# Performance work log

Hardware: AMD Instinct MI355X
Metric: run time of the kernel (lower is better)

The kernel has to match this reference:

```python
import jax, jax.numpy as jnp
import numpy as np

DIM = 256  # channel width
B, H, W = 4, 64, 64


def conv2d(x, w, b, pad, groups=1):
    # x: NCHW, w: OIHW (I = C_in/groups)
    y = jax.lax.conv_general_dilated(
        x, w, window_strides=(1, 1),
        padding=[(pad[0], pad[0]), (pad[1], pad[1])],
        dimension_numbers=("NCHW", "OIHW", "NCHW"),
        feature_group_count=groups)
    return y + b[None, :, None, None]


def l2norm(x, eps=1e-12):
    # matches F.normalize(x, dim=-1): x / max(||x||_2, eps)
    n = jnp.sqrt(jnp.sum(x * x, axis=-1, keepdims=True))
    return x / jnp.maximum(n, eps)


def setup_inputs() -> dict:
    key = jax.random.key(0)
    ks = jax.random.split(key, 12)
    dim, c8 = DIM, DIM // 8
    w = lambda k, shape, s: jax.random.normal(k, shape, jnp.float32) * s
    return {
        "x": jax.random.normal(ks[0], (B, dim, H, W), jnp.float32),
        "w_conv": w(ks[1], (dim, dim, 3, 3), 0.02), "b_conv": jnp.zeros((dim,), jnp.float32),
        "w01": w(ks[2], (dim, 1, 1, 7), 0.05), "b01": jnp.zeros((dim,), jnp.float32),
        "w02": w(ks[3], (dim, 1, 7, 1), 0.05), "b02": jnp.zeros((dim,), jnp.float32),
        "w11": w(ks[4], (dim, 1, 1, 11), 0.05), "b11": jnp.zeros((dim,), jnp.float32),
        "w12": w(ks[5], (dim, 1, 11, 1), 0.05), "b12": jnp.zeros((dim,), jnp.float32),
        "w21": w(ks[6], (dim, 1, 1, 21), 0.05), "b21": jnp.zeros((dim,), jnp.float32),
        "w22": w(ks[7], (dim, 1, 21, 1), 0.05), "b22": jnp.zeros((dim,), jnp.float32),
        "w_proj": w(ks[8], (c8, dim, 1, 1), 0.05), "b_proj": jnp.zeros((c8,), jnp.float32),
        "w3": w(ks[9], (c8, dim // 4, 1, 1), 0.05), "b3": jnp.zeros((c8,), jnp.float32),
        "w4": w(ks[10], (dim, c8, 1, 1), 0.05), "b4": jnp.zeros((dim,), jnp.float32),
    }


def reference(x, w_conv, b_conv, w01, b01, w02, b02, w11, b11, w12, b12,
              w21, b21, w22, b22, w_proj, b_proj, w3, b3, w4, b4):
    b, c, h, w_ = x.shape
    x = conv2d(x, w_conv, b_conv, (1, 1))
    # multi-scale separable depthwise convs (7, 11, 21)
    x1 = conv2d(conv2d(x, w01, b01, (0, 3), c), w02, b02, (3, 0), c)
    x2 = conv2d(conv2d(x, w11, b11, (0, 5), c), w12, b12, (5, 0), c)
    x3 = conv2d(conv2d(x, w21, b21, (0, 10), c), w22, b22, (10, 0), c)
    out1 = x1 + x2 + x3 + x                      # [b, dim, h, w]
    out1 = conv2d(out1, w_proj, b_proj, (0, 0))  # [b, dim//8, h, w]
    c8 = out1.shape[1]
    t = out1.reshape(b, c8, h * w_)              # b head c (h w), head=1

    q1 = l2norm(t)
    attn1 = jax.nn.softmax(q1 @ jnp.swapaxes(q1, -2, -1), axis=-1)  # [b, c8, c8]
    out2 = attn1 @ t                                                # [b, c8, hw]

    # branch 2: spatial attention (hw x hw)
    ts = jnp.swapaxes(t, -2, -1)                 # [b, hw, c8]
    q2 = l2norm(ts)
    attn2 = jax.nn.softmax(q2 @ jnp.swapaxes(q2, -2, -1), axis=-1)  # [b, hw, hw]
    out3 = jnp.swapaxes(attn2 @ ts, -2, -1)                         # [b, c8, hw]

    out4 = jnp.concatenate([out2.reshape(b, c8, h, w_),
                            out3.reshape(b, c8, h, w_)], axis=1)    # [b, dim//4, h, w]
    out5 = conv2d(out4, w3, b3, (0, 0)) + out1
    return conv2d(out5, w4, b4, (0, 0))          # [b, dim, h, w]
```

## Files before the change

kernel.cpp:

```cpp
#include <hip/hip_runtime.h>
#include <hip/hip_bf16.h>

typedef __hip_bfloat16 bf16;
typedef short s16;
typedef __attribute__((ext_vector_type(4))) short s16x4;
typedef __attribute__((ext_vector_type(8))) short s16x8;
typedef __attribute__((ext_vector_type(4))) float f32x4;

__device__ __forceinline__ s16 f2b(float f){
    unsigned u = __float_as_uint(f);
    unsigned r = (u + 0x7FFFu + ((u >> 16) & 1u)) >> 16;
    return (s16)r;
}
__device__ __forceinline__ float b2f_bits(s16 v){
    return __uint_as_float(((unsigned)(unsigned short)v) << 16);
}

__global__ __launch_bounds__(256) void prep_k(const float* __restrict__ x, s16* __restrict__ xcl,
                                              const float* __restrict__ w, s16* __restrict__ wpk){
    __shared__ s16 lb[64][258];
    int blk = blockIdx.x, t = threadIdx.x;
    if (blk < 256){
        int h = blk & 63, b = blk >> 6;
        for (int i = t; i < 16384; i += 256){
            int ci = i >> 6, ww = i & 63;
            lb[ww][ci] = f2b(x[((b*256 + ci)*64 + h)*64 + ww]);
        }
        __syncthreads();
        for (int i = t; i < 16384; i += 256){
            int ww = i >> 8, ci = i & 255;
            xcl[(b*4096 + h*64 + ww)*256 + ci] = lb[ww][ci];
        }
    } else {
        int base = (blk - 256)*1024 + t;
        #pragma unroll
        for (int k = 0; k < 4; ++k){
            int idx = base + k*256;
            int cil = idx & 31;
            int r   = idx >> 5;
            int co  = r & 255;
            int r2  = r >> 8;
            int tap = r2 % 9, cc = r2 / 9;
            wpk[idx] = f2b(w[(co*256 + cc*32 + cil)*9 + tap]);
        }
    }
}

__global__ __launch_bounds__(256) void conv3x3m_k(const s16* __restrict__ xcl,
        const s16* __restrict__ wpk, const float* __restrict__ bias,
        bf16* __restrict__ y0){
    __shared__ alignas(16) s16 smem[30240];
    s16* xls = smem;
    s16* wls = smem + 9504;
    const int sp = blockIdx.x, cog = blockIdx.y;
    const int b = sp >> 5, h0 = (sp & 31)*2;
    const int t = threadIdx.x;
    const int wv = t >> 6, lane = t & 63;
    const int lm = lane & 15, g = lane >> 4;

    f32x4 acc[2][4];
    #pragma unroll
    for (int mi = 0; mi < 2; ++mi)
        #pragma unroll
        for (int ni = 0; ni < 4; ++ni) acc[mi][ni] = (f32x4){0.f,0.f,0.f,0.f};

    for (int cc = 0; cc < 8; ++cc){
        __syncthreads();
        for (int i = t; i < 1056; i += 256){
            int g8 = i & 3, wi = (i>>2) % 66, r = (i>>2) / 66;
            int h = h0 - 1 + r, w = wi - 1;
            s16x8 v = {0,0,0,0,0,0,0,0};
            if (h >= 0 && h < 64 && w >= 0 && w < 64)
                v = *(const s16x8*)&xcl[(b*4096 + h*64 + w)*256 + cc*32 + g8*8];
            s16* d = &xls[(r*66 + wi)*36 + g8*8];
            *(s16x4*)d       = __builtin_shufflevector(v, v, 0,1,2,3);
            *(s16x4*)(d + 4) = __builtin_shufflevector(v, v, 4,5,6,7);
        }
        for (int i = t; i < 2304; i += 256){
            int g8 = i & 3, co = (i>>2) & 63, tap = i >> 8;
            s16x8 v = *(const s16x8*)&wpk[((cc*9 + tap)*256 + cog*64 + co)*32 + g8*8];
            s16* d = &wls[(tap*64 + co)*36 + g8*8];
            *(s16x4*)d       = __builtin_shufflevector(v, v, 0,1,2,3);
            *(s16x4*)(d + 4) = __builtin_shufflevector(v, v, 4,5,6,7);
        }
        __syncthreads();
        #pragma unroll
        for (int tap = 0; tap < 9; ++tap){
            const int kh = tap/3, kw = tap%3;
            s16x8 bfr[4], afr[2];
            #pragma unroll
            for (int ni = 0; ni < 4; ++ni){
                const s16* p = &wls[(tap*64 + ni*16 + lm)*36 + g*8];
                s16x4 lo = *(const s16x4*)p;
                s16x4 hi = *(const s16x4*)(p + 4);
                bfr[ni] = __builtin_shufflevector(lo, hi, 0,1,2,3,4,5,6,7);
            }
            #pragma unroll
            for (int mi = 0; mi < 2; ++mi){
                int m = (wv*2 + mi)*16 + lm;
                int hr = m >> 6, ww = m & 63;
                const s16* p = &xls[((hr + kh)*66 + (ww + kw))*36 + g*8];
                s16x4 lo = *(const s16x4*)p;
                s16x4 hi = *(const s16x4*)(p + 4);
                afr[mi] = __builtin_shufflevector(lo, hi, 0,1,2,3,4,5,6,7);
            }
            #pragma unroll
            for (int mi = 0; mi < 2; ++mi)
                #pragma unroll
                for (int ni = 0; ni < 4; ++ni)
                    acc[mi][ni] = __builtin_amdgcn_mfma_f32_16x16x32_bf16(
                        afr[mi], bfr[ni], acc[mi][ni], 0, 0, 0);
        }
    }
    __syncthreads();
    float* ot = (float*)smem;
    #pragma unroll
    for (int mi = 0; mi < 2; ++mi)
        #pragma unroll
        for (int ni = 0; ni < 4; ++ni)
            #pragma unroll
            for (int r = 0; r < 4; ++r){
                int m  = (wv*2 + mi)*16 + g*4 + r;
                int co = ni*16 + lm;
                ot[co*132 + m] = acc[mi][ni][r];
            }
    __syncthreads();
    for (int i = t; i < 8192; i += 256){
        int co = i >> 7, m = i & 127;
        float v = ot[co*132 + m] + bias[cog*64 + co];
        y0[((b*256 + cog*64 + co)*64 + h0 + (m>>6))*64 + (m & 63)] = __float2bfloat16(v);
    }
}

template<int K>
__device__ __forceinline__ void sep_branch(const float (*__restrict__ pl)[65], float (*__restrict__ hp)[65],
                                           int c, int t,
                                           const float* __restrict__ wh, const float* __restrict__ bh,
                                           const float* __restrict__ wv, const float* __restrict__ bv,
                                           float* acc){
    constexpr int P = K/2;
    constexpr int W = 16 + 2*P;
    float wk[K];
    #pragma unroll
    for (int j = 0; j < K; ++j) wk[j] = wh[c*K + j];
    float bhv = bh[c];
    {
        int h = t >> 2, w0 = (t & 3)*16;
        float win[W];
        #pragma unroll
        for (int j = 0; j < W; ++j){
            int ww = w0 - P + j;
            win[j] = (ww >= 0 && ww < 64) ? pl[h][ww] : 0.f;
        }
        __syncthreads();
        #pragma unroll
        for (int i = 0; i < 16; ++i){
            float s = bhv;
            #pragma unroll
            for (int k = 0; k < K; ++k) s += win[i+k]*wk[k];
            hp[h][w0 + i] = s;
        }
    }
    float vk[K];
    #pragma unroll
    for (int j = 0; j < K; ++j) vk[j] = wv[c*K + j];
    float bvv = bv[c];
    __syncthreads();
    {
        int w = t & 63, h0 = (t >> 6)*16;
        float win[W];
        #pragma unroll
        for (int j = 0; j < W; ++j){
            int hh = h0 - P + j;
            win[j] = (hh >= 0 && hh < 64) ? hp[hh][w] : 0.f;
        }
        #pragma unroll
        for (int i = 0; i < 16; ++i){
            float s = bvv;
            #pragma unroll
            for (int k = 0; k < K; ++k) s += win[i+k]*vk[k];
            acc[i] += s;
        }
    }
}

__global__ __launch_bounds__(256) void sepconv_k(const bf16* __restrict__ y0,
        const float* __restrict__ w01, const float* __restrict__ b01,
        const float* __restrict__ w02, const float* __restrict__ b02,
        const float* __restrict__ w11, const float* __restrict__ b11,
        const float* __restrict__ w12, const float* __restrict__ b12,
        const float* __restrict__ w21, const float* __restrict__ b21,
        const float* __restrict__ w22, const float* __restrict__ b22,
        bf16* __restrict__ out1){
    __shared__ float pl[64][65];
    __shared__ float hp[64][65];
    int bc = blockIdx.x;
    int c = bc & 255;
    int t = threadIdx.x;
    const s16* src = (const s16*)(y0 + bc*4096);
    #pragma unroll
    for (int k = 0; k < 2; ++k){
        int chunk = t + k*256;
        int h = chunk >> 3, w8 = (chunk & 7)*8;
        s16x8 v = *(const s16x8*)&src[h*64 + w8];
        #pragma unroll
        for (int e = 0; e < 8; ++e) pl[h][w8 + e] = b2f_bits(v[e]);
    }
    __syncthreads();
    float acc[16];
    #pragma unroll
    for (int k = 0; k < 16; ++k) acc[k] = 0.f;
    sep_branch<7 >(pl, hp, c, t, w01, b01, w02, b02, acc);
    sep_branch<11>(pl, hp, c, t, w11, b11, w12, b12, acc);
    sep_branch<21>(pl, hp, c, t, w21, b21, w22, b22, acc);
    __syncthreads();
    {
        int w = t & 63, h0 = (t >> 6)*16;
        #pragma unroll
        for (int i = 0; i < 16; ++i) hp[h0 + i][w] = acc[i] + pl[h0 + i][w];
    }
    __syncthreads();
    s16* dst = (s16*)(out1 + bc*4096);
    #pragma unroll
    for (int k = 0; k < 2; ++k){
        int chunk = t + k*256;
        int h = chunk >> 3, w8 = (chunk & 7)*8;
        s16x8 o;
        #pragma unroll
        for (int e = 0; e < 8; ++e) o[e] = f2b(hp[h][w8 + e]);
        *(s16x8*)&dst[h*64 + w8] = o;
    }
}

__global__ __launch_bounds__(256) void proj_k(const bf16* __restrict__ out1, const float* __restrict__ wp,
                                              const float* __restrict__ bp,
                                              s16* __restrict__ tTb, float* __restrict__ rn2){
    __shared__ float wl[256*32];
    __shared__ s16 part[4][64][36];
    int pt = blockIdx.x, b = blockIdx.y, t = threadIdx.x;
    int q = t >> 6, lane = t & 63;
    for (int i = t; i < 8192; i += 256){
        int ci = i >> 5, cc = i & 31;
        wl[ci*32 + cc] = wp[cc*256 + ci];
    }
    __syncthreads();
    int p = pt*64 + lane;
    float acc[32] = {};
    const bf16* xb = out1 + b*1048576 + p;
    for (int ci = q*64; ci < q*64 + 64; ++ci){
        float v = __bfloat162float(xb[ci*4096]);
        const float* wr = &wl[ci*32];
        #pragma unroll
        for (int c8 = 0; c8 < 8; ++c8){
            float4 w4 = *(const float4*)&wr[c8*4];
            acc[c8*4+0] += w4.x*v; acc[c8*4+1] += w4.y*v;
            acc[c8*4+2] += w4.z*v; acc[c8*4+3] += w4.w*v;
        }
    }
    #pragma unroll
    for (int cc = 0; cc < 32; ++cc) part[q][lane][cc] = f2b(acc[cc]);
    __syncthreads();
    int p_loc = t >> 2, qq = t & 3;
    int pg = pt*64 + p_loc;
    float a8[8];
    float ss = 0.f;
    #pragma unroll
    for (int c = 0; c < 8; ++c){
        int cc = qq*8 + c;
        float v = b2f_bits(part[0][p_loc][cc]) + b2f_bits(part[1][p_loc][cc])
                + b2f_bits(part[2][p_loc][cc]) + b2f_bits(part[3][p_loc][cc]) + bp[cc];
        a8[c] = v;
        ss += v*v;
    }
    ss += __shfl_xor(ss, 1, 4);
    ss += __shfl_xor(ss, 2, 4);
    if (qq == 0) rn2[b*4096 + pg] = 1.f / fmaxf(sqrtf(ss), 1e-12f);
    s16x8 o8;
    #pragma unroll
    for (int c = 0; c < 8; ++c) o8[c] = f2b(a8[c]);
    *(s16x8*)&tTb[(b*4096 + pg)*32 + qq*8] = o8;
}

__global__ __launch_bounds__(256) void gramm_k(const s16* __restrict__ tTb, float* __restrict__ part){
    __shared__ alignas(16) s16 ts[32*268];
    int ks = blockIdx.x, b = blockIdx.y, t = threadIdx.x;
    {
        const s16* src = &tTb[(b*4096 + ks*256 + t)*32];
        s16 row[32];
        #pragma unroll
        for (int q = 0; q < 4; ++q){
            s16x8 v = *(const s16x8*)&src[q*8];
            #pragma unroll
            for (int e = 0; e < 8; ++e) row[q*8 + e] = v[e];
        }
        #pragma unroll
        for (int cc = 0; cc < 32; ++cc) ts[cc*268 + t] = row[cc];
    }
    __syncthreads();
    int wv = t >> 6, lane = t & 63, lm = lane & 15, g = lane >> 4;
    int mi = wv >> 1, ni = wv & 1;
    f32x4 acc = (f32x4){0.f,0.f,0.f,0.f};
    const s16* ar = &ts[(mi*16 + lm)*268];
    const s16* br = &ts[(ni*16 + lm)*268];
    #pragma unroll
    for (int kk = 0; kk < 8; ++kk){
        const s16* ap = ar + kk*32 + g*8;
        s16x4 alo = *(const s16x4*)ap;
        s16x4 ahi = *(const s16x4*)(ap + 4);
        s16x8 af = __builtin_shufflevector(alo, ahi, 0,1,2,3,4,5,6,7);
        const s16* bp = br + kk*32 + g*8;
        s16x4 blo = *(const s16x4*)bp;
        s16x4 bhi = *(const s16x4*)(bp + 4);
        s16x8 bf = __builtin_shufflevector(blo, bhi, 0,1,2,3,4,5,6,7);
        acc = __builtin_amdgcn_mfma_f32_16x16x32_bf16(af, bf, acc, 0, 0, 0);
    }
    float* pd = part + (b*16 + ks)*1024;
    #pragma unroll
    for (int r = 0; r < 4; ++r){
        int i = mi*16 + g*4 + r, j = ni*16 + lm;
        pd[i*32 + j] = acc[r];
    }
}

__global__ __launch_bounds__(256) void afold_k(const float* __restrict__ part,
        const float* __restrict__ w3, const float* __restrict__ b3,
        const float* __restrict__ w4, const float* __restrict__ b4,
        float* __restrict__ WtT, float* __restrict__ WoT, float* __restrict__ bfo){
    __shared__ float rn[32];
    __shared__ float rsum[32];
    __shared__ float a1[1024];
    __shared__ float w3a[1024];
    __shared__ float w3bs[1024];
    int b = blockIdx.x, t = threadIdx.x;
    if (t < 32){
        float gjj = 0.f;
        #pragma unroll 8
        for (int ps = 0; ps < 16; ++ps) gjj += part[(b*16+ps)*1024 + t*33];
        rn[t] = 1.f / fmaxf(sqrtf(gjj), 1e-12f);
    }
    for (int idx = t; idx < 1024; idx += 256){
        int i = idx >> 5, j = idx & 31;
        w3bs[idx] = w3[i*64 + 32 + j];
    }
    __syncthreads();
    for (int e = t; e < 1024; e += 256){
        int i = e >> 5, j = e & 31;
        float gij = 0.f;
        #pragma unroll 8
        for (int ps = 0; ps < 16; ++ps) gij += part[(b*16+ps)*1024 + e];
        a1[e] = __expf(rn[i]*rn[j]*gij);
    }
    __syncthreads();
    if (t < 32){
        float s = 0.f;
        #pragma unroll 8
        for (int j = 0; j < 32; ++j) s += a1[t*32 + j];
        rsum[t] = 1.f / s;
    }
    __syncthreads();
    for (int e = t; e < 1024; e += 256) a1[e] *= rsum[e >> 5];
    __syncthreads();
    for (int idx = t; idx < 1024; idx += 256){
        int cc = idx >> 5, j = idx & 31;
        float s = 0.f;
        #pragma unroll 8
        for (int i = 0; i < 32; ++i) s += w3[cc*64 + i]*a1[i*32 + j];
        w3a[idx] = s;
    }
    __syncthreads();
    int co = t;
    float w4r[32];
    #pragma unroll
    for (int cc = 0; cc < 32; ++cc) w4r[cc] = w4[co*32 + cc];
    float bfv = b4[co];
    #pragma unroll
    for (int cc = 0; cc < 32; ++cc) bfv += w4r[cc]*b3[cc];
    bfo[b*256 + co] = bfv;
    for (int j = 0; j < 32; ++j){
        float st = w4r[j];
        float so = 0.f;
        #pragma unroll 8
        for (int cc = 0; cc < 32; ++cc){
            st += w4r[cc]*w3a[cc*32 + j];
            so += w4r[cc]*w3bs[cc*32 + j];
        }
        WtT[(b*32 + j)*256 + co] = st;
        WoT[(b*32 + j)*256 + co] = so;
    }
}

__global__ __launch_bounds__(256) void flashm_k(const s16* __restrict__ tTb, const float* __restrict__ rn2,
                                                float* __restrict__ partA, float* __restrict__ partL){
    __shared__ alignas(16) s16 kvb[128*36];
    __shared__ alignas(16) s16 vts[32*132];
    __shared__ alignas(16) s16 pls[4][16*132];
    __shared__ float rnj[128];
    __shared__ float ri[64];
    const int ib = blockIdx.x, b = blockIdx.y, chunk = blockIdx.z;
    const int t = threadIdx.x, wv = t >> 6, lane = t & 63;
    const int lm = lane & 15, g = lane >> 4;
    const int i0 = ib*64;

    if (t < 64) ri[t] = rn2[b*4096 + i0 + t];
    s16x8 qf = *(const s16x8*)&tTb[(b*4096 + i0 + wv*16 + lm)*32 + g*8];
    __syncthreads();
    float rni4[4];
    #pragma unroll
    for (int r = 0; r < 4; ++r) rni4[r] = ri[wv*16 + g*4 + r];

    f32x4 oacc[2];
    oacc[0] = (f32x4){0.f,0.f,0.f,0.f};
    oacc[1] = (f32x4){0.f,0.f,0.f,0.f};
    float lacc[4] = {0.f,0.f,0.f,0.f};
    s16* pw = pls[wv];

    for (int jt = chunk*8; jt < chunk*8 + 8; ++jt){
        const int j0 = jt*128;
        __syncthreads();
        for (int gi = t; gi < 512; gi += 256){
            int j = gi >> 2, g8 = gi & 3;
            s16x8 v = *(const s16x8*)&tTb[(b*4096 + j0 + j)*32 + g8*8];
            s16* d = &kvb[j*36 + g8*8];
            *(s16x4*)d       = __builtin_shufflevector(v, v, 0,1,2,3);
            *(s16x4*)(d + 4) = __builtin_shufflevector(v, v, 4,5,6,7);
            #pragma unroll
            for (int e = 0; e < 8; ++e) vts[(g8*8 + e)*132 + j] = v[e];
        }
        if (t < 128) rnj[t] = rn2[b*4096 + j0 + t];
        __syncthreads();
        #pragma unroll
        for (int nt = 0; nt < 8; ++nt){
            const s16* bp = &kvb[(nt*16 + lm)*36 + g*8];
            s16x4 blo = *(const s16x4*)bp;
            s16x4 bhi = *(const s16x4*)(bp + 4);
            s16x8 bf = __builtin_shufflevector(blo, bhi, 0,1,2,3,4,5,6,7);
            f32x4 s = __builtin_amdgcn_mfma_f32_16x16x32_bf16(qf, bf,
                        (f32x4){0.f,0.f,0.f,0.f}, 0, 0, 0);
            float rj = rnj[nt*16 + lm];
            #pragma unroll
            for (int r = 0; r < 4; ++r){
                float e = __expf(s[r]*rni4[r]*rj);
                lacc[r] += e;
                pw[(g*4 + r)*132 + nt*16 + lm] = f2b(e);
            }
        }
        #pragma unroll
        for (int ks = 0; ks < 4; ++ks){
            const s16* ap = &pw[lm*132 + ks*32 + g*8];
            s16x4 alo = *(const s16x4*)ap;
            s16x4 ahi = *(const s16x4*)(ap + 4);
            s16x8 af = __builtin_shufflevector(alo, ahi, 0,1,2,3,4,5,6,7);
            #pragma unroll
            for (int n2 = 0; n2 < 2; ++n2){
                const s16* vp = &vts[(n2*16 + lm)*132 + ks*32 + g*8];
                s16x4 vlo = *(const s16x4*)vp;
                s16x4 vhi = *(const s16x4*)(vp + 4);
                s16x8 vf = __builtin_shufflevector(vlo, vhi, 0,1,2,3,4,5,6,7);
                oacc[n2] = __builtin_amdgcn_mfma_f32_16x16x32_bf16(af, vf, oacc[n2], 0, 0, 0);
            }
        }
    }
    #pragma unroll
    for (int r = 0; r < 4; ++r){
        float v = lacc[r];
        v += __shfl_xor(v, 1, 16); v += __shfl_xor(v, 2, 16);
        v += __shfl_xor(v, 4, 16); v += __shfl_xor(v, 8, 16);
        lacc[r] = v;
    }
    const int base = (b*4 + chunk)*4096 + i0 + wv*16;
    #pragma unroll
    for (int n2 = 0; n2 < 2; ++n2)
        #pragma unroll
        for (int r = 0; r < 4; ++r)
            partA[(base + g*4 + r)*32 + n2*16 + lm] = oacc[n2][r];
    if (lm == 0){
        #pragma unroll
        for (int r = 0; r < 4; ++r) partL[base + g*4 + r] = lacc[r];
    }
}

__global__ __launch_bounds__(256) void finalfuse_k(const s16* __restrict__ tTb,
        const float* __restrict__ partA, const float* __restrict__ partL,
        const float* __restrict__ WtT, const float* __restrict__ WoT,
        const float* __restrict__ bfo, float* __restrict__ out){
    int pt = blockIdx.x, cog = blockIdx.y, b = blockIdx.z, t = threadIdx.x;
    int p = pt*256 + t;
    float l = 0.f;
    #pragma unroll
    for (int c = 0; c < 4; ++c) l += partL[(b*4 + c)*4096 + p];
    float inv = 1.f / l;
    float v3[32];
    #pragma unroll
    for (int q = 0; q < 8; ++q){
        float4 s0 = *(const float4*)&partA[((b*4 + 0)*4096 + p)*32 + q*4];
        float4 s1 = *(const float4*)&partA[((b*4 + 1)*4096 + p)*32 + q*4];
        float4 s2 = *(const float4*)&partA[((b*4 + 2)*4096 + p)*32 + q*4];
        float4 s3 = *(const float4*)&partA[((b*4 + 3)*4096 + p)*32 + q*4];
        v3[q*4+0] = (s0.x + s1.x + s2.x + s3.x)*inv;
        v3[q*4+1] = (s0.y + s1.y + s2.y + s3.y)*inv;
        v3[q*4+2] = (s0.z + s1.z + s2.z + s3.z)*inv;
        v3[q*4+3] = (s0.w + s1.w + s2.w + s3.w)*inv;
    }
    float vt[32];
    {
        const s16* tp = &tTb[(b*4096 + p)*32];
        #pragma unroll
        for (int q = 0; q < 4; ++q){
            s16x8 v = *(const s16x8*)&tp[q*8];
            #pragma unroll
            for (int e = 0; e < 8; ++e) vt[q*8 + e] = b2f_bits(v[e]);
        }
    }
    float acc[32];
    #pragma unroll
    for (int co = 0; co < 32; ++co) acc[co] = bfo[b*256 + cog*32 + co];
    for (int j = 0; j < 32; ++j){
        float vtj = vt[j];
        float vo  = v3[j];
        const float* wtr = WtT + (b*32 + j)*256 + cog*32;
        const float* wor = WoT + (b*32 + j)*256 + cog*32;
        #pragma unroll
        for (int co = 0; co < 32; ++co) acc[co] += wtr[co]*vtj + wor[co]*vo;
    }
    #pragma unroll
    for (int co = 0; co < 32; ++co)
        out[((b*256 + cog*32 + co)*4096) + p] = acc[co];
}

extern "C" void kernel_launch(void* const* d_in, const int* in_sizes, int n_in,
                              void* d_out, int out_size, void* d_ws, size_t ws_size,
                              hipStream_t stream) {
    const float* x      = (const float*)d_in[0];
    const float* w_conv = (const float*)d_in[1];
    const float* b_conv = (const float*)d_in[2];
    const float* w01 = (const float*)d_in[3];  const float* b01 = (const float*)d_in[4];
    const float* w02 = (const float*)d_in[5];  const float* b02 = (const float*)d_in[6];
    const float* w11 = (const float*)d_in[7];  const float* b11 = (const float*)d_in[8];
    const float* w12 = (const float*)d_in[9];  const float* b12 = (const float*)d_in[10];
    const float* w21 = (const float*)d_in[11]; const float* b21 = (const float*)d_in[12];
    const float* w22 = (const float*)d_in[13]; const float* b22 = (const float*)d_in[14];
    const float* w_proj = (const float*)d_in[15]; const float* b_proj = (const float*)d_in[16];
    const float* w3 = (const float*)d_in[17]; const float* b3 = (const float*)d_in[18];
    const float* w4 = (const float*)d_in[19]; const float* b4 = (const float*)d_in[20];

    char* wsb = (char*)d_ws;
    s16*   xcl  = (s16*)wsb;
    bf16*  out1 = (bf16*)wsb;
    bf16*  y0   = (bf16*)(wsb + 8388608);
    s16*   wpk  = (s16*)(wsb + 16777216);
    float* f    = (float*)d_ws;
    float* part   = f + 0;
    float* partA  = f + 0;
    s16*   tTb    = (s16*)(wsb + 10485760);
    float* WtT    = f + 3145728;
    float* WoT    = f + 3178496;
    float* bfo    = f + 3211264;
    float* partL  = f + 4194304;
    float* rn2    = f + 4726912;

    prep_k<<<dim3(832), 256, 0, stream>>>(x, xcl, w_conv, wpk);
    conv3x3m_k<<<dim3(128, 4), 256, 0, stream>>>(xcl, wpk, b_conv, y0);
    sepconv_k<<<dim3(1024), 256, 0, stream>>>(y0, w01, b01, w02, b02,
                                              w11, b11, w12, b12,
                                              w21, b21, w22, b22, out1);
    proj_k<<<dim3(64, 4), 256, 0, stream>>>(out1, w_proj, b_proj, tTb, rn2);
    gramm_k<<<dim3(16, 4), 256, 0, stream>>>(tTb, part);
    afold_k<<<dim3(4), 256, 0, stream>>>(part, w3, b3, w4, b4, WtT, WoT, bfo);
    flashm_k<<<dim3(64, 4, 4), 256, 0, stream>>>(tTb, rn2, partA, partL);
    finalfuse_k<<<dim3(16, 8, 4), 256, 0, stream>>>(tTb, partA, partL, WtT, WoT, bfo,
                                                    (float*)d_out);
}
```

Measured before the change: 297.1 us.

## Pre-pad conv input in global memory and read A fragments directly

Measured after the change: 305.9 us. +2.9%, slower.

```diff
diff --git a/kernel.cpp b/kernel.cpp
--- a/kernel.cpp
+++ b/kernel.cpp
@@ -16,7 +16,7 @@
     return __uint_as_float(((unsigned)(unsigned short)v) << 16);
 }
 
-__global__ __launch_bounds__(256) void prep_k(const float* __restrict__ x, s16* __restrict__ xcl,
+__global__ __launch_bounds__(256) void prep_k(const float* __restrict__ x, s16* __restrict__ xclp,
                                               const float* __restrict__ w, s16* __restrict__ wpk){
     __shared__ s16 lb[64][258];
     int blk = blockIdx.x, t = threadIdx.x;
@@ -29,7 +29,7 @@
         __syncthreads();
         for (int i = t; i < 16384; i += 256){
             int ww = i >> 8, ci = i & 255;
-            xcl[(b*4096 + h*64 + ww)*256 + ci] = lb[ww][ci];
+            xclp[((b*66 + h + 1)*66 + ww + 1)*256 + ci] = lb[ww][ci];
         }
     } else {
         int base = (blk - 256)*1024 + t;
@@ -46,12 +46,10 @@
     }
 }
 
-__global__ __launch_bounds__(256) void conv3x3m_k(const s16* __restrict__ xcl,
+__global__ __launch_bounds__(256) void conv3x3m_k(const s16* __restrict__ xclp,
         const s16* __restrict__ wpk, const float* __restrict__ bias,
         bf16* __restrict__ y0){
-    __shared__ alignas(16) s16 smem[30240];
-    s16* xls = smem;
-    s16* wls = smem + 9504;
+    __shared__ alignas(16) s16 smem[20736];
     const int sp = blockIdx.x, cog = blockIdx.y;
     const int b = sp >> 5, h0 = (sp & 31)*2;
     const int t = threadIdx.x;
@@ -64,46 +62,36 @@
         #pragma unroll
         for (int ni = 0; ni < 4; ++ni) acc[mi][ni] = (f32x4){0.f,0.f,0.f,0.f};
 
+    const int m0 = (wv*2 + 0)*16 + lm, m1 = (wv*2 + 1)*16 + lm;
+    const int hr0 = m0 >> 6, ww0 = m0 & 63;
+    const int hr1 = m1 >> 6, ww1 = m1 & 63;
+
     for (int cc = 0; cc < 8; ++cc){
         __syncthreads();
-        for (int i = t; i < 1056; i += 256){
-            int g8 = i & 3, wi = (i>>2) % 66, r = (i>>2) / 66;
-            int h = h0 - 1 + r, w = wi - 1;
-            s16x8 v = {0,0,0,0,0,0,0,0};
-            if (h >= 0 && h < 64 && w >= 0 && w < 64)
-                v = *(const s16x8*)&xcl[(b*4096 + h*64 + w)*256 + cc*32 + g8*8];
-            s16* d = &xls[(r*66 + wi)*36 + g8*8];
-            *(s16x4*)d       = __builtin_shufflevector(v, v, 0,1,2,3);
-            *(s16x4*)(d + 4) = __builtin_shufflevector(v, v, 4,5,6,7);
-        }
         for (int i = t; i < 2304; i += 256){
             int g8 = i & 3, co = (i>>2) & 63, tap = i >> 8;
             s16x8 v = *(const s16x8*)&wpk[((cc*9 + tap)*256 + cog*64 + co)*32 + g8*8];
-            s16* d = &wls[(tap*64 + co)*36 + g8*8];
+            s16* d = &smem[(tap*64 + co)*36 + g8*8];
             *(s16x4*)d       = __builtin_shufflevector(v, v, 0,1,2,3);
             *(s16x4*)(d + 4) = __builtin_shufflevector(v, v, 4,5,6,7);
         }
         __syncthreads();
+        const s16* a0 = xclp + (((b*66 + h0 + hr0)*66 + ww0)*256 + cc*32 + g*8);
+        const s16* a1 = xclp + (((b*66 + h0 + hr1)*66 + ww1)*256 + cc*32 + g*8);
         #pragma unroll
         for (int tap = 0; tap < 9; ++tap){
             const int kh = tap/3, kw = tap%3;
+            const int aoff = (kh*66 + kw)*256;
             s16x8 bfr[4], afr[2];
             #pragma unroll
             for (int ni = 0; ni < 4; ++ni){
-                const s16* p = &wls[(tap*64 + ni*16 + lm)*36 + g*8];
+                const s16* p = &smem[(tap*64 + ni*16 + lm)*36 + g*8];
                 s16x4 lo = *(const s16x4*)p;
                 s16x4 hi = *(const s16x4*)(p + 4);
                 bfr[ni] = __builtin_shufflevector(lo, hi, 0,1,2,3,4,5,6,7);
             }
-            #pragma unroll
-            for (int mi = 0; mi < 2; ++mi){
-                int m = (wv*2 + mi)*16 + lm;
-                int hr = m >> 6, ww = m & 63;
-                const s16* p = &xls[((hr + kh)*66 + (ww + kw))*36 + g*8];
-                s16x4 lo = *(const s16x4*)p;
-                s16x4 hi = *(const s16x4*)(p + 4);
-                afr[mi] = __builtin_shufflevector(lo, hi, 0,1,2,3,4,5,6,7);
-            }
+            afr[0] = *(const s16x8*)(a0 + aoff);
+            afr[1] = *(const s16x8*)(a1 + aoff);
             #pragma unroll
             for (int mi = 0; mi < 2; ++mi)
                 #pragma unroll
@@ -544,10 +532,10 @@
     const float* w4 = (const float*)d_in[19]; const float* b4 = (const float*)d_in[20];
 
     char* wsb = (char*)d_ws;
-    s16*   xcl  = (s16*)wsb;
+    s16*   xclp = (s16*)wsb;
     bf16*  out1 = (bf16*)wsb;
-    bf16*  y0   = (bf16*)(wsb + 8388608);
-    s16*   wpk  = (s16*)(wsb + 16777216);
+    bf16*  y0   = (bf16*)(wsb + 8921088);
+    s16*   wpk  = (s16*)(wsb + 17309696);
     float* f    = (float*)d_ws;
     float* part   = f + 0;
     float* partA  = f + 0;
@@ -558,8 +546,9 @@
     float* partL  = f + 4194304;
     float* rn2    = f + 4726912;
 
-    prep_k<<<dim3(832), 256, 0, stream>>>(x, xcl, w_conv, wpk);
-    conv3x3m_k<<<dim3(128, 4), 256, 0, stream>>>(xcl, wpk, b_conv, y0);
+    hipMemsetAsync(xclp, 0, 8921088, stream);
+    prep_k<<<dim3(832), 256, 0, stream>>>(x, xclp, w_conv, wpk);
+    conv3x3m_k<<<dim3(128, 4), 256, 0, stream>>>(xclp, wpk, b_conv, y0);
     sepconv_k<<<dim3(1024), 256, 0, stream>>>(y0, w01, b01, w02, b02,
                                               w11, b11, w12, b12,
                                               w21, b21, w22, b22, out1);
```
